# Kernel optimization log

Measured on AMD Instinct MI355X. Metric: run time of the kernel, lower is better.

Reference implementation:

```python
import jax, jax.numpy as jnp
import numpy as np

B, S, I, H, O = 64, 512, 256, 1024, 256


def setup_inputs() -> dict:
    key = jax.random.key(0)
    ks = jax.random.split(key, 12)
    s_in = 1.0 / np.sqrt(H)  # torch RNN init scale
    inp = {
        "x": jax.random.normal(ks[0], (B, S, I), dtype=jnp.float32),
        "W_ih_0": jax.random.uniform(ks[1], (H, I), jnp.float32, -s_in, s_in),
        "W_hh_0": jax.random.uniform(ks[2], (H, H), jnp.float32, -s_in, s_in),
        "b_ih_0": jax.random.uniform(ks[3], (H,), jnp.float32, -s_in, s_in),
        "b_hh_0": jax.random.uniform(ks[4], (H,), jnp.float32, -s_in, s_in),
        "W_ih_1": jax.random.uniform(ks[5], (H, H), jnp.float32, -s_in, s_in),
        "W_hh_1": jax.random.uniform(ks[6], (H, H), jnp.float32, -s_in, s_in),
        "b_ih_1": jax.random.uniform(ks[7], (H,), jnp.float32, -s_in, s_in),
        "b_hh_1": jax.random.uniform(ks[8], (H,), jnp.float32, -s_in, s_in),
        "fc_w": jax.random.uniform(ks[9], (O, H), jnp.float32, -s_in, s_in),
        "fc_b": jax.random.uniform(ks[10], (O,), jnp.float32, -s_in, s_in),
    }
    return inp


def _rnn_layer(inp, W_ih, W_hh, b_ih, b_hh):
    # Pre-compute input projection for all timesteps (one big GEMM),
    # then scan the sequential recurrence: h_t = tanh(Wx_t + U h_{t-1} + b)
    pre = jnp.einsum('bsi,hi->bsh', inp, W_ih) + (b_ih + b_hh)  # [B,S,H]
    h0 = jnp.zeros((inp.shape[0], W_hh.shape[0]), dtype=inp.dtype)

    def step(h, p_t):
        h = jnp.tanh(p_t + h @ W_hh.T)
        return h, h

    _, hs = jax.lax.scan(step, h0, jnp.swapaxes(pre, 0, 1))  # [S,B,H]
    return jnp.swapaxes(hs, 0, 1)  # [B,S,H]


def reference(x, W_ih_0, W_hh_0, b_ih_0, b_hh_0,
              W_ih_1, W_hh_1, b_ih_1, b_hh_1, fc_w, fc_b):
    h = _rnn_layer(x, W_ih_0, W_hh_0, b_ih_0, b_hh_0)
    h = _rnn_layer(h, W_ih_1, W_hh_1, b_ih_1, b_hh_1)
    return h @ fc_w.T + fc_b  # [B,S,O]
```

## Files before the change

kernel.cpp:

```cpp
#include <hip/hip_runtime.h>
#include <hip/hip_bf16.h>


typedef __attribute__((ext_vector_type(4))) float f32x4;
typedef __attribute__((ext_vector_type(8))) short bf16x8;
typedef __attribute__((ext_vector_type(4))) int   i32x4;
typedef __attribute__((ext_vector_type(4))) short s16x4;

#define B_  64
#define S_  512
#define I_  256
#define H_  1024
#define O_  256
#define M_  (B_ * S_)
#define SH_ (S_ * H_)

static __device__ __forceinline__ unsigned short f2bf(float f) {
  union { float f; unsigned u; } v; v.f = f;
  unsigned r = v.u + 0x7fffu + ((v.u >> 16) & 1u);
  return (unsigned short)(r >> 16);
}

static __device__ __forceinline__ float tanh_fast(float x) {
  float e = __expf(2.f * x);
  return 1.f - 2.f / (e + 1.f);
}

__global__ void cvt_bf16(const float* __restrict__ src,
                         unsigned short* __restrict__ dst, int n4) {
  int i = blockIdx.x * blockDim.x + threadIdx.x;
  if (i < n4) {
    f32x4 v = ((const f32x4*)src)[i];
    s16x4 o;
    o[0] = (short)f2bf(v[0]); o[1] = (short)f2bf(v[1]);
    o[2] = (short)f2bf(v[2]); o[3] = (short)f2bf(v[3]);
    ((s16x4*)dst)[i] = o;
  }
}

__global__ __launch_bounds__(256)
void gemm_bf16(const unsigned short* __restrict__ A,
               const unsigned short* __restrict__ W,
               const float* __restrict__ b1, const float* __restrict__ b2,
               float* __restrict__ C, int Mx, int Nx, int Kx) {
  __shared__ __align__(16) unsigned short As[128 * 40];
  __shared__ __align__(16) unsigned short Bs[128 * 40];
  const int tid  = threadIdx.x;
  const int m0   = blockIdx.y * 128;
  const int n0   = blockIdx.x * 128;
  const int w    = tid >> 6, lane = tid & 63;
  const int quad = lane >> 4, l15 = lane & 15;
  const int wm = (w & 1) * 64, wn = (w >> 1) * 64;

  f32x4 acc[4][4] = {};

  for (int k0 = 0; k0 < Kx; k0 += 32) {
#pragma unroll
    for (int i = 0; i < 2; ++i) {
      int c = tid + i * 256;
      int row = c >> 2, kc = c & 3;
      *(i32x4*)&As[row * 40 + kc * 8] =
          *(const i32x4*)&A[(size_t)(m0 + row) * Kx + k0 + kc * 8];
      *(i32x4*)&Bs[row * 40 + kc * 8] =
          *(const i32x4*)&W[(size_t)(n0 + row) * Kx + k0 + kc * 8];
    }
    __syncthreads();
    bf16x8 af[4], bg[4];
#pragma unroll
    for (int im = 0; im < 4; ++im)
      af[im] = *(const bf16x8*)&As[(wm + im * 16 + l15) * 40 + quad * 8];
#pragma unroll
    for (int in = 0; in < 4; ++in)
      bg[in] = *(const bf16x8*)&Bs[(wn + in * 16 + l15) * 40 + quad * 8];
#pragma unroll
    for (int im = 0; im < 4; ++im)
#pragma unroll
      for (int in = 0; in < 4; ++in)
        acc[im][in] = __builtin_amdgcn_mfma_f32_16x16x32_bf16(
            af[im], bg[in], acc[im][in], 0, 0, 0);
    __syncthreads();
  }

#pragma unroll
  for (int in = 0; in < 4; ++in) {
    int n = n0 + wn + in * 16 + l15;
    float bv = b1[n];
    if (b2) bv += b2[n];
#pragma unroll
    for (int im = 0; im < 4; ++im) {
      int mb = m0 + wm + im * 16 + quad * 4;
#pragma unroll
      for (int r = 0; r < 4; ++r)
        C[(size_t)(mb + r) * Nx + n] = acc[im][in][r] + bv;
    }
  }
}

__global__ __launch_bounds__(256, 1)
void rnn_persist(const unsigned short* __restrict__ Whh,
                 const float* __restrict__ pre,
                 unsigned short* __restrict__ hseq,
                 unsigned int* __restrict__ flags)
{
  const int bx   = blockIdx.x;
  const int g    = bx >> 4;
  const int j    = bx & 15;
  const int n0   = j * 64;
  const int tid  = threadIdx.x;
  const int w    = tid >> 6;
  const int lane = tid & 63;
  const int quad = lane >> 4, l15 = lane & 15;

  __shared__ __align__(16) float q[4][4][16][20];

  bf16x8 Wf[4][8];
  {
    const unsigned short* wp = Whh + (size_t)(n0 + l15) * H_ + w * 256 + quad * 8;
#pragma unroll
    for (int i = 0; i < 4; ++i)
#pragma unroll
      for (int kk = 0; kk < 8; ++kk)
        Wf[i][kk] = *(const bf16x8*)(wp + (size_t)i * 16 * H_ + kk * 32);
  }

  unsigned int* const gflag = flags + g * S_;

  for (int t = 0; t < S_; ++t) {
    float pv[4];
#pragma unroll
    for (int r = 0; r < 4; ++r)
      pv[r] = pre[(size_t)(g * 16 + quad * 4 + r) * SH_ + (size_t)t * H_ +
                  n0 + w * 16 + l15];

    f32x4 acc[4] = {};

    if (t > 0) {
      if (tid == 0) {
        while (__hip_atomic_load(&gflag[t - 1], __ATOMIC_RELAXED,
                                 __HIP_MEMORY_SCOPE_AGENT) < 16u) {}
        __builtin_amdgcn_fence(__ATOMIC_ACQUIRE, "agent");
      }
      __syncthreads();

      const unsigned short* hp = hseq + (size_t)(g * 16 + l15) * SH_ +
                                 (size_t)(t - 1) * H_ + w * 256 + quad * 8;
      bf16x8 Af[8];
#pragma unroll
      for (int kk = 0; kk < 8; ++kk)
        Af[kk] = *(const bf16x8*)(hp + kk * 32);
#pragma unroll
      for (int kk = 0; kk < 8; ++kk)
#pragma unroll
        for (int i = 0; i < 4; ++i)
          acc[i] = __builtin_amdgcn_mfma_f32_16x16x32_bf16(
              Af[kk], Wf[i][kk], acc[i], 0, 0, 0);
    }

#pragma unroll
    for (int i = 0; i < 4; ++i)
      *(f32x4*)&q[w][i][l15][quad * 4] = acc[i];
    __syncthreads();

    f32x4 s = {};
#pragma unroll
    for (int wp2 = 0; wp2 < 4; ++wp2) {
      f32x4 v = *(const f32x4*)&q[wp2][w][l15][quad * 4];
#pragma unroll
      for (int r = 0; r < 4; ++r) s[r] += v[r];
    }

#pragma unroll
    for (int r = 0; r < 4; ++r) {
      float xv = pv[r] + s[r];
      unsigned short hb = f2bf(tanh_fast(xv));
      size_t o = (size_t)(g * 16 + quad * 4 + r) * SH_ + (size_t)t * H_ +
                 n0 + w * 16 + l15;
      __hip_atomic_store(&hseq[o], hb, __ATOMIC_RELAXED,
                         __HIP_MEMORY_SCOPE_AGENT);
    }
    __syncthreads();
    if (tid == 0)
      __hip_atomic_fetch_add(&gflag[t], 1u, __ATOMIC_RELAXED,
                             __HIP_MEMORY_SCOPE_AGENT);
  }
}

extern "C" void kernel_launch(void* const* d_in, const int* in_sizes, int n_in,
                              void* d_out, int out_size, void* d_ws, size_t ws_size,
                              hipStream_t stream) {
  const float* x      = (const float*)d_in[0];
  const float* W_ih_0 = (const float*)d_in[1];
  const float* W_hh_0 = (const float*)d_in[2];
  const float* b_ih_0 = (const float*)d_in[3];
  const float* b_hh_0 = (const float*)d_in[4];
  const float* W_ih_1 = (const float*)d_in[5];
  const float* W_hh_1 = (const float*)d_in[6];
  const float* b_ih_1 = (const float*)d_in[7];
  const float* b_hh_1 = (const float*)d_in[8];
  const float* fc_w   = (const float*)d_in[9];
  const float* fc_b   = (const float*)d_in[10];
  float* out = (float*)d_out;

  char* ws = (char*)d_ws;
  size_t off = 0;
  auto alloc = [&](size_t bytes) { char* p = ws + off; off += (bytes + 255) & ~(size_t)255; return p; };
  unsigned short* xb    = (unsigned short*)alloc((size_t)M_ * I_ * 2);
  unsigned short* wih0b = (unsigned short*)alloc((size_t)H_ * I_ * 2);
  unsigned short* whh0b = (unsigned short*)alloc((size_t)H_ * H_ * 2);
  unsigned short* wih1b = (unsigned short*)alloc((size_t)H_ * H_ * 2);
  unsigned short* whh1b = (unsigned short*)alloc((size_t)H_ * H_ * 2);
  unsigned short* fcwb  = (unsigned short*)alloc((size_t)O_ * H_ * 2);
  unsigned int*   flags = (unsigned int*)alloc(2 * 4 * S_ * 4);
  float*          pre   = (float*)alloc((size_t)M_ * H_ * 4);
  unsigned short* h0seq = (unsigned short*)alloc((size_t)M_ * H_ * 2);
  unsigned short* h1seq;
  if (off + (size_t)M_ * H_ * 2 <= ws_size)
    h1seq = (unsigned short*)alloc((size_t)M_ * H_ * 2);
  else
    h1seq = h0seq;

  hipMemsetAsync(flags, 0, 2 * 4 * S_ * 4, stream);

  auto cvt = [&](const float* s, unsigned short* d, int n) {
    int n4 = n / 4;
    cvt_bf16<<<(n4 + 255) / 256, 256, 0, stream>>>(s, d, n4);
  };
  cvt(x,      xb,    M_ * I_);
  cvt(W_ih_0, wih0b, H_ * I_);
  cvt(W_hh_0, whh0b, H_ * H_);
  cvt(W_ih_1, wih1b, H_ * H_);
  cvt(W_hh_1, whh1b, H_ * H_);
  cvt(fc_w,   fcwb,  O_ * H_);

  gemm_bf16<<<dim3(H_ / 128, M_ / 128), 256, 0, stream>>>(
      xb, wih0b, b_ih_0, b_hh_0, pre, M_, H_, I_);
  rnn_persist<<<64, 256, 0, stream>>>(whh0b, pre, h0seq, flags);

  gemm_bf16<<<dim3(H_ / 128, M_ / 128), 256, 0, stream>>>(
      h0seq, wih1b, b_ih_1, b_hh_1, pre, M_, H_, H_);
  rnn_persist<<<64, 256, 0, stream>>>(whh1b, pre, h1seq, flags + 4 * S_);

  gemm_bf16<<<dim3(O_ / 128, M_ / 128), 256, 0, stream>>>(
      h1seq, fcwb, fc_b, nullptr, out, M_, O_, H_);
}
```

Before: 3.263 ms.

## Fuse both RNN layers into one wavefront-pipelined persistent kernel

Runs layer 0 and layer 1 recurrences concurrently in one persistent kernel of 128 blocks. Layer-1 blocks compute the input projection on the fly from h0 at step t, using register-resident W_ih_1, and wait on layer-0 flags. This removes the separate layer-1 input GEMM and its large fp32 pre buffer, and overlaps the two sequential scans. The layer-0 pre-activations are also stored as bf16 to halve their traffic, which costs precision. It also drops the barrier before h loads so every thread spins on the flag, and doubles register use for layer-1 blocks.

```diff
diff --git a/kernel.cpp b/kernel.cpp
--- a/kernel.cpp
+++ b/kernel.cpp
@@ -20,7 +20,10 @@
   unsigned r = v.u + 0x7fffu + ((v.u >> 16) & 1u);
   return (unsigned short)(r >> 16);
 }
-
+static __device__ __forceinline__ float bf2f(unsigned short b) {
+  union { unsigned u; float f; } v; v.u = ((unsigned)b) << 16;
+  return v.f;
+}
 static __device__ __forceinline__ float tanh_fast(float x) {
   float e = __expf(2.f * x);
   return 1.f - 2.f / (e + 1.f);
@@ -38,11 +41,12 @@
   }
 }
 
+template <bool BF16OUT>
 __global__ __launch_bounds__(256)
 void gemm_bf16(const unsigned short* __restrict__ A,
                const unsigned short* __restrict__ W,
                const float* __restrict__ b1, const float* __restrict__ b2,
-               float* __restrict__ C, int Mx, int Nx, int Kx) {
+               void* __restrict__ Cv, int Mx, int Nx, int Kx) {
   __shared__ __align__(16) unsigned short As[128 * 40];
   __shared__ __align__(16) unsigned short Bs[128 * 40];
   const int tid  = threadIdx.x;
@@ -84,28 +88,38 @@
 #pragma unroll
   for (int in = 0; in < 4; ++in) {
     int n = n0 + wn + in * 16 + l15;
-    float bv = b1[n];
+    float bv = b1 ? b1[n] : 0.f;
     if (b2) bv += b2[n];
 #pragma unroll
     for (int im = 0; im < 4; ++im) {
       int mb = m0 + wm + im * 16 + quad * 4;
 #pragma unroll
-      for (int r = 0; r < 4; ++r)
-        C[(size_t)(mb + r) * Nx + n] = acc[im][in][r] + bv;
+      for (int r = 0; r < 4; ++r) {
+        float val = acc[im][in][r] + bv;
+        size_t o = (size_t)(mb + r) * Nx + n;
+        if (BF16OUT) ((unsigned short*)Cv)[o] = f2bf(val);
+        else         ((float*)Cv)[o] = val;
+      }
     }
   }
 }
 
 __global__ __launch_bounds__(256, 1)
-void rnn_persist(const unsigned short* __restrict__ Whh,
-                 const float* __restrict__ pre,
-                 unsigned short* __restrict__ hseq,
-                 unsigned int* __restrict__ flags)
+void rnn_fused(const unsigned short* __restrict__ Whh0,
+               const unsigned short* __restrict__ Wih1,
+               const unsigned short* __restrict__ Whh1,
+               const unsigned short* __restrict__ pre0,
+               const float* __restrict__ b_ih_1,
+               const float* __restrict__ b_hh_1,
+               unsigned short* __restrict__ h0seq,
+               unsigned short* __restrict__ h1seq,
+               unsigned int* __restrict__ flags)
 {
   const int bx   = blockIdx.x;
-  const int g    = bx >> 4;
-  const int j    = bx & 15;
-  const int n0   = j * 64;
+  const int L    = bx >> 6;
+  const int id   = bx & 63;
+  const int g    = id >> 4;
+  const int n0   = (id & 15) * 64;
   const int tid  = threadIdx.x;
   const int w    = tid >> 6;
   const int lane = tid & 63;
@@ -113,75 +127,148 @@
 
   __shared__ __align__(16) float q[4][4][16][20];
 
-  bf16x8 Wf[4][8];
-  {
-    const unsigned short* wp = Whh + (size_t)(n0 + l15) * H_ + w * 256 + quad * 8;
-#pragma unroll
-    for (int i = 0; i < 4; ++i)
-#pragma unroll
-      for (int kk = 0; kk < 8; ++kk)
-        Wf[i][kk] = *(const bf16x8*)(wp + (size_t)i * 16 * H_ + kk * 32);
-  }
-
-  unsigned int* const gflag = flags + g * S_;
-
-  for (int t = 0; t < S_; ++t) {
-    float pv[4];
-#pragma unroll
-    for (int r = 0; r < 4; ++r)
-      pv[r] = pre[(size_t)(g * 16 + quad * 4 + r) * SH_ + (size_t)t * H_ +
-                  n0 + w * 16 + l15];
-
-    f32x4 acc[4] = {};
-
-    if (t > 0) {
-      if (tid == 0) {
-        while (__hip_atomic_load(&gflag[t - 1], __ATOMIC_RELAXED,
+  unsigned int* const f0 = flags + g * S_;
+  unsigned int* const f1 = flags + 4 * S_ + g * S_;
+
+  if (L == 0) {
+    bf16x8 Wf[4][8];
+    {
+      const unsigned short* wp = Whh0 + (size_t)(n0 + l15) * H_ + w * 256 + quad * 8;
+#pragma unroll
+      for (int i = 0; i < 4; ++i)
+#pragma unroll
+        for (int kk = 0; kk < 8; ++kk)
+          Wf[i][kk] = *(const bf16x8*)(wp + (size_t)i * 16 * H_ + kk * 32);
+    }
+
+    for (int t = 0; t < S_; ++t) {
+      float pv[4];
+      {
+        const unsigned short* pp = pre0 + (size_t)(g * 16 + quad * 4) * SH_ +
+                                   (size_t)t * H_ + n0 + w * 16 + l15;
+#pragma unroll
+        for (int r = 0; r < 4; ++r) pv[r] = bf2f(pp[(size_t)r * SH_]);
+      }
+
+      f32x4 acc[4] = {};
+      if (t > 0) {
+        while (__hip_atomic_load(&f0[t - 1], __ATOMIC_RELAXED,
                                  __HIP_MEMORY_SCOPE_AGENT) < 16u) {}
         __builtin_amdgcn_fence(__ATOMIC_ACQUIRE, "agent");
-      }
+        const unsigned short* hp = h0seq + (size_t)(g * 16 + l15) * SH_ +
+                                   (size_t)(t - 1) * H_ + w * 256 + quad * 8;
+        bf16x8 Af[8];
+#pragma unroll
+        for (int kk = 0; kk < 8; ++kk) Af[kk] = *(const bf16x8*)(hp + kk * 32);
+#pragma unroll
+        for (int kk = 0; kk < 8; ++kk)
+#pragma unroll
+          for (int i = 0; i < 4; ++i)
+            acc[i] = __builtin_amdgcn_mfma_f32_16x16x32_bf16(
+                Af[kk], Wf[i][kk], acc[i], 0, 0, 0);
+      }
+
+#pragma unroll
+      for (int i = 0; i < 4; ++i) *(f32x4*)&q[w][i][l15][quad * 4] = acc[i];
       __syncthreads();
-
-      const unsigned short* hp = hseq + (size_t)(g * 16 + l15) * SH_ +
-                                 (size_t)(t - 1) * H_ + w * 256 + quad * 8;
-      bf16x8 Af[8];
-#pragma unroll
-      for (int kk = 0; kk < 8; ++kk)
-        Af[kk] = *(const bf16x8*)(hp + kk * 32);
-#pragma unroll
-      for (int kk = 0; kk < 8; ++kk)
-#pragma unroll
-        for (int i = 0; i < 4; ++i)
-          acc[i] = __builtin_amdgcn_mfma_f32_16x16x32_bf16(
-              Af[kk], Wf[i][kk], acc[i], 0, 0, 0);
-    }
-
-#pragma unroll
-    for (int i = 0; i < 4; ++i)
-      *(f32x4*)&q[w][i][l15][quad * 4] = acc[i];
-    __syncthreads();
-
-    f32x4 s = {};
-#pragma unroll
-    for (int wp2 = 0; wp2 < 4; ++wp2) {
-      f32x4 v = *(const f32x4*)&q[wp2][w][l15][quad * 4];
-#pragma unroll
-      for (int r = 0; r < 4; ++r) s[r] += v[r];
-    }
-
-#pragma unroll
-    for (int r = 0; r < 4; ++r) {
-      float xv = pv[r] + s[r];
-      unsigned short hb = f2bf(tanh_fast(xv));
-      size_t o = (size_t)(g * 16 + quad * 4 + r) * SH_ + (size_t)t * H_ +
-                 n0 + w * 16 + l15;
-      __hip_atomic_store(&hseq[o], hb, __ATOMIC_RELAXED,
-                         __HIP_MEMORY_SCOPE_AGENT);
-    }
-    __syncthreads();
-    if (tid == 0)
-      __hip_atomic_fetch_add(&gflag[t], 1u, __ATOMIC_RELAXED,
-                             __HIP_MEMORY_SCOPE_AGENT);
+      f32x4 s = {};
+#pragma unroll
+      for (int wp2 = 0; wp2 < 4; ++wp2) {
+        f32x4 v = *(const f32x4*)&q[wp2][w][l15][quad * 4];
+#pragma unroll
+        for (int r = 0; r < 4; ++r) s[r] += v[r];
+      }
+
+#pragma unroll
+      for (int r = 0; r < 4; ++r) {
+        unsigned short hb = f2bf(tanh_fast(pv[r] + s[r]));
+        size_t o = (size_t)(g * 16 + quad * 4 + r) * SH_ + (size_t)t * H_ +
+                   n0 + w * 16 + l15;
+        __hip_atomic_store(&h0seq[o], hb, __ATOMIC_RELAXED,
+                           __HIP_MEMORY_SCOPE_AGENT);
+      }
+      __syncthreads();
+      if (tid == 0)
+        __hip_atomic_fetch_add(&f0[t], 1u, __ATOMIC_RELAXED,
+                               __HIP_MEMORY_SCOPE_AGENT);
+    }
+  } else {
+    bf16x8 Wi[4][8], Wr[4][8];
+    {
+      const unsigned short* wpi = Wih1 + (size_t)(n0 + l15) * H_ + w * 256 + quad * 8;
+      const unsigned short* wpr = Whh1 + (size_t)(n0 + l15) * H_ + w * 256 + quad * 8;
+#pragma unroll
+      for (int i = 0; i < 4; ++i)
+#pragma unroll
+        for (int kk = 0; kk < 8; ++kk) {
+          Wi[i][kk] = *(const bf16x8*)(wpi + (size_t)i * 16 * H_ + kk * 32);
+          Wr[i][kk] = *(const bf16x8*)(wpr + (size_t)i * 16 * H_ + kk * 32);
+        }
+    }
+    const int ncol = n0 + w * 16 + l15;
+    const float bias = b_ih_1[ncol] + b_hh_1[ncol];
+
+    for (int t = 0; t < S_; ++t) {
+      f32x4 acc[4] = {};
+
+      if (t > 0) {
+        while (__hip_atomic_load(&f1[t - 1], __ATOMIC_RELAXED,
+                                 __HIP_MEMORY_SCOPE_AGENT) < 16u) {}
+        __builtin_amdgcn_fence(__ATOMIC_ACQUIRE, "agent");
+        const unsigned short* hp = h1seq + (size_t)(g * 16 + l15) * SH_ +
+                                   (size_t)(t - 1) * H_ + w * 256 + quad * 8;
+        bf16x8 Af[8];
+#pragma unroll
+        for (int kk = 0; kk < 8; ++kk) Af[kk] = *(const bf16x8*)(hp + kk * 32);
+#pragma unroll
+        for (int kk = 0; kk < 8; ++kk)
+#pragma unroll
+          for (int i = 0; i < 4; ++i)
+            acc[i] = __builtin_amdgcn_mfma_f32_16x16x32_bf16(
+                Af[kk], Wr[i][kk], acc[i], 0, 0, 0);
+      }
+
+      {
+        while (__hip_atomic_load(&f0[t], __ATOMIC_RELAXED,
+                                 __HIP_MEMORY_SCOPE_AGENT) < 16u) {}
+        __builtin_amdgcn_fence(__ATOMIC_ACQUIRE, "agent");
+        const unsigned short* hp = h0seq + (size_t)(g * 16 + l15) * SH_ +
+                                   (size_t)t * H_ + w * 256 + quad * 8;
+        bf16x8 Af[8];
+#pragma unroll
+        for (int kk = 0; kk < 8; ++kk) Af[kk] = *(const bf16x8*)(hp + kk * 32);
+#pragma unroll
+        for (int kk = 0; kk < 8; ++kk)
+#pragma unroll
+          for (int i = 0; i < 4; ++i)
+            acc[i] = __builtin_amdgcn_mfma_f32_16x16x32_bf16(
+                Af[kk], Wi[i][kk], acc[i], 0, 0, 0);
+      }
+
+#pragma unroll
+      for (int i = 0; i < 4; ++i) *(f32x4*)&q[w][i][l15][quad * 4] = acc[i];
+      __syncthreads();
+      f32x4 s = {};
+#pragma unroll
+      for (int wp2 = 0; wp2 < 4; ++wp2) {
+        f32x4 v = *(const f32x4*)&q[wp2][w][l15][quad * 4];
+#pragma unroll
+        for (int r = 0; r < 4; ++r) s[r] += v[r];
+      }
+
+#pragma unroll
+      for (int r = 0; r < 4; ++r) {
+        unsigned short hb = f2bf(tanh_fast(bias + s[r]));
+        size_t o = (size_t)(g * 16 + quad * 4 + r) * SH_ + (size_t)t * H_ +
+                   n0 + w * 16 + l15;
+        __hip_atomic_store(&h1seq[o], hb, __ATOMIC_RELAXED,
+                           __HIP_MEMORY_SCOPE_AGENT);
+      }
+      __syncthreads();
+      if (tid == 0)
+        __hip_atomic_fetch_add(&f1[t], 1u, __ATOMIC_RELAXED,
+                               __HIP_MEMORY_SCOPE_AGENT);
+    }
   }
 }
 
@@ -211,13 +298,9 @@
   unsigned short* whh1b = (unsigned short*)alloc((size_t)H_ * H_ * 2);
   unsigned short* fcwb  = (unsigned short*)alloc((size_t)O_ * H_ * 2);
   unsigned int*   flags = (unsigned int*)alloc(2 * 4 * S_ * 4);
-  float*          pre   = (float*)alloc((size_t)M_ * H_ * 4);
+  unsigned short* pre0b = (unsigned short*)alloc((size_t)M_ * H_ * 2);
   unsigned short* h0seq = (unsigned short*)alloc((size_t)M_ * H_ * 2);
-  unsigned short* h1seq;
-  if (off + (size_t)M_ * H_ * 2 <= ws_size)
-    h1seq = (unsigned short*)alloc((size_t)M_ * H_ * 2);
-  else
-    h1seq = h0seq;
+  unsigned short* h1seq = (unsigned short*)alloc((size_t)M_ * H_ * 2);
 
   hipMemsetAsync(flags, 0, 2 * 4 * S_ * 4, stream);
 
@@ -232,14 +315,12 @@
   cvt(W_hh_1, whh1b, H_ * H_);
   cvt(fc_w,   fcwb,  O_ * H_);
 
-  gemm_bf16<<<dim3(H_ / 128, M_ / 128), 256, 0, stream>>>(
-      xb, wih0b, b_ih_0, b_hh_0, pre, M_, H_, I_);
-  rnn_persist<<<64, 256, 0, stream>>>(whh0b, pre, h0seq, flags);
-
-  gemm_bf16<<<dim3(H_ / 128, M_ / 128), 256, 0, stream>>>(
-      h0seq, wih1b, b_ih_1, b_hh_1, pre, M_, H_, H_);
-  rnn_persist<<<64, 256, 0, stream>>>(whh1b, pre, h1seq, flags + 4 * S_);
-
-  gemm_bf16<<<dim3(O_ / 128, M_ / 128), 256, 0, stream>>>(
+  gemm_bf16<true><<<dim3(H_ / 128, M_ / 128), 256, 0, stream>>>(
+      xb, wih0b, b_ih_0, b_hh_0, pre0b, M_, H_, I_);
+
+  rnn_fused<<<128, 256, 0, stream>>>(whh0b, wih1b, whh1b, pre0b,
+                                     b_ih_1, b_hh_1, h0seq, h1seq, flags);
+
+  gemm_bf16<false><<<dim3(O_ / 128, M_ / 128), 256, 0, stream>>>(
       h1seq, fcwb, fc_b, nullptr, out, M_, O_, H_);
 }
```

New measurement: 4.199 ms. 1.29x slower.
